# Performance work log

Hardware: AMD Instinct MI355X
Metric: run time of the kernel (lower is better)

## Reference

```python
import jax, jax.numpy as jnp
import numpy as np

B, T, IN = 64, 512, 3      # batch, stroke timesteps, stroke features
H = 512                    # hidden_dim
K = 10                     # num_gaussian_window
NC = 80                    # num_chars
U = 64                     # char_seq_len


def setup_inputs() -> dict:
    key = jax.random.key(0)
    ks = jax.random.split(key, 8)
    w = lambda k, sh: (jax.random.normal(k, sh, jnp.float32) * 0.05)
    return {
        "strokes": jax.random.normal(ks[0], (B, T, IN), jnp.float32),
        "sentences": jax.random.randint(ks[1], (B, U), 0, NC),
        "sentences_mask": jnp.ones((B, U), jnp.float32),
        # nn.LSTMCell params (gate order i, f, g, o)
        "W_ih": w(ks[2], (4 * H, IN + NC)),
        "W_hh": w(ks[3], (4 * H, H)),
        "b_ih": w(ks[4], (4 * H,)),
        "b_hh": w(ks[5], (4 * H,)),
        # window_layer: Linear(H, 3K)
        "W_win": w(ks[6], (3 * K, H)),
        "b_win": w(ks[7], (3 * K,)),
    }


def reference(strokes, sentences, sentences_mask, W_ih, W_hh, b_ih, b_hh, W_win, b_win):
    Bsz, Tlen, _ = strokes.shape
    Ulen = sentences.shape[-1]
    Hh = W_hh.shape[1]
    Kg = W_win.shape[0] // 3
    NCc = W_ih.shape[1] - strokes.shape[-1]
    dt = strokes.dtype

    # one_hot(sentences) * mask, precomputed once: [B, U, NC]
    C = jax.nn.one_hot(sentences, NCc, dtype=dt) * sentences_mask[..., None]
    u = jnp.arange(Ulen, dtype=dt)  # [U]

    def step(carry, x_t):
        h, c, kappa, w = carry
        inp = jnp.concatenate([x_t, w], axis=-1)              # [B, IN+NC]
        gates = inp @ W_ih.T + b_ih + h @ W_hh.T + b_hh       # [B, 4H]
        i, f, g, o = jnp.split(gates, 4, axis=-1)
        c = jax.nn.sigmoid(f) * c + jax.nn.sigmoid(i) * jnp.tanh(g)
        h = jax.nn.sigmoid(o) * jnp.tanh(c)
        p = h @ W_win.T + b_win                               # [B, 3K]
        a_hat, b_hat, k_hat = jnp.split(p, 3, axis=-1)
        alpha = jnp.exp(a_hat)
        beta = jnp.exp(b_hat)
        kappa = kappa + jnp.exp(k_hat)
        # phi[b,u] = sum_k alpha * exp(-beta * (kappa - u)^2)
        phi = jnp.einsum(
            "bk,bku->bu", alpha,
            jnp.exp(-beta[..., None] * (kappa[..., None] - u) ** 2))
        w = jnp.einsum("bu,bun->bn", phi, C)                  # [B, NC]
        return (h, c, kappa, w), (h, w)

    init = (
        jnp.zeros((Bsz, Hh), dt),
        jnp.zeros((Bsz, Hh), dt),
        jnp.zeros((Bsz, Kg), dt),
        jnp.zeros((Bsz, NCc), dt),
    )
    _, (hs, ws) = jax.lax.scan(step, init, jnp.swapaxes(strokes, 0, 1))
    # time-major -> batch-major: [B, T, H], [B, T, NC]
    return jnp.swapaxes(hs, 0, 1), jnp.swapaxes(ws, 0, 1)
```

## Files before the change

### kernel.cpp

```cpp
#include <hip/hip_runtime.h>
#include <hip/hip_bf16.h>


#define GRID_BLOCKS 64
#define TPB 256

typedef __attribute__((ext_vector_type(8))) __bf16 bf16x8;
typedef __attribute__((ext_vector_type(4))) float f32x4;
typedef __attribute__((ext_vector_type(2))) float f32x2;

struct Smem {
    alignas(16) __bf16 wBf[64 * 104];
    float P[64 * 33];
    float Gt[64 * 33];
    float Al[640];
    float Be[640];
    float Ka[640];
    float Wacc[64 * 80];
    float Xt[192];
    float Maskv[4096];
    float Wx[96];
    float Bsum[32];
    float Bwin[32];
    int   Act[64];
    unsigned char Sent[4096];
};

__device__ __forceinline__ float sigf(float x) {
    return 1.f / (1.f + __expf(-x));
}
__device__ __forceinline__ float tanh_fast(float x) {
    float xx = fminf(fmaxf(x, -15.f), 15.f);
    float e = __expf(2.f * xx);
    return (e - 1.f) / (e + 1.f);
}

__global__ void init_ws_kernel(int* ws) {
    int idx = blockIdx.x * TPB + threadIdx.x;
    if (idx < 32832) ws[idx] = 0;
}

__global__ void __launch_bounds__(TPB, 1) lstm_attn(
    const float* __restrict__ strokes,
    const int*   __restrict__ sentences,
    const float* __restrict__ smask,
    const float* __restrict__ Wih,
    const float* __restrict__ Whh,
    const float* __restrict__ bih,
    const float* __restrict__ bhh,
    const float* __restrict__ Wwin,
    const float* __restrict__ bwin,
    float* __restrict__ out,
    unsigned short* __restrict__ hbuf,
    int* __restrict__ flags)
{
    __shared__ Smem S;
    const int tid  = threadIdx.x;
    const int blk  = blockIdx.x;
    const int lane = tid & 63;
    const int wave = tid >> 6;
    const int lm   = lane & 15;
    const int quad = lane >> 4;
    const int myb  = wave * 16 + lm;
    const int koff = quad * 8;
    volatile int* vflags = (volatile int*)flags;

    bf16x8 rbG[2][19];
    bf16x8 rbP[2][16];
    #pragma unroll
    for (int tau = 0; tau < 2; ++tau) {
        const int colg = (lm >> 2) * 512 + blk * 8 + tau * 4 + (lm & 3);
        const float* wr = Whh + colg * 512;
        #pragma unroll
        for (int kc = 0; kc < 16; ++kc) {
            f32x4 lo = *(const f32x4*)(wr + kc * 32 + koff);
            f32x4 hi = *(const f32x4*)(wr + kc * 32 + koff + 4);
            bf16x8 b;
            b[0] = (__bf16)lo[0]; b[1] = (__bf16)lo[1];
            b[2] = (__bf16)lo[2]; b[3] = (__bf16)lo[3];
            b[4] = (__bf16)hi[0]; b[5] = (__bf16)hi[1];
            b[6] = (__bf16)hi[2]; b[7] = (__bf16)hi[3];
            rbG[tau][kc] = b;
        }
        #pragma unroll
        for (int kc = 0; kc < 3; ++kc) {
            bf16x8 b;
            #pragma unroll
            for (int j = 0; j < 8; ++j) {
                int k = kc * 32 + koff + j;
                b[j] = (__bf16)((k < 80) ? Wih[colg * 83 + 3 + k] : 0.f);
            }
            rbG[tau][16 + kc] = b;
        }
    }
    #pragma unroll
    for (int nt = 0; nt < 2; ++nt) {
        const int r = nt * 16 + lm;
        #pragma unroll
        for (int kc = 0; kc < 16; ++kc) {
            bf16x8 b;
            if (r < 30) {
                f32x4 lo = *(const f32x4*)(Wwin + r * 512 + kc * 32 + koff);
                f32x4 hi = *(const f32x4*)(Wwin + r * 512 + kc * 32 + koff + 4);
                b[0] = (__bf16)lo[0]; b[1] = (__bf16)lo[1];
                b[2] = (__bf16)lo[2]; b[3] = (__bf16)lo[3];
                b[4] = (__bf16)hi[0]; b[5] = (__bf16)hi[1];
                b[6] = (__bf16)hi[2]; b[7] = (__bf16)hi[3];
            } else {
                #pragma unroll
                for (int j = 0; j < 8; ++j) b[j] = (__bf16)0.f;
            }
            rbP[nt][kc] = b;
        }
    }

    for (int idx = tid; idx < 4096; idx += TPB) {
        S.Sent[idx]  = (unsigned char)sentences[idx];
        S.Maskv[idx] = smask[idx];
    }
    if (tid < 32) {
        int tau = tid >> 4, m = tid & 15;
        int colg = (m >> 2) * 512 + blk * 8 + tau * 4 + (m & 3);
        S.Bsum[tid] = bih[colg] + bhh[colg];
        S.Wx[tid * 3 + 0] = Wih[colg * 83 + 0];
        S.Wx[tid * 3 + 1] = Wih[colg * 83 + 1];
        S.Wx[tid * 3 + 2] = Wih[colg * 83 + 2];
        S.Bwin[tid] = (tid < 30) ? bwin[tid] : 0.f;
    }
    for (int idx = tid; idx < 640; idx += TPB) S.Ka[idx] = 0.f;
    for (int idx = tid; idx < 5120; idx += TPB) S.Wacc[idx] = 0.f;
    for (int idx = tid; idx < 64 * 104; idx += TPB) S.wBf[idx] = (__bf16)0.f;
    float cst0 = 0.f, cst1 = 0.f;
    __syncthreads();

    const float bs0 = S.Bsum[lm], bs1 = S.Bsum[16 + lm];
    const float bw0 = S.Bwin[lm], bw1 = S.Bwin[16 + lm];
    float wx[6];
    #pragma unroll
    for (int m = 0; m < 3; ++m) {
        wx[m]     = S.Wx[lm * 3 + m];
        wx[3 + m] = S.Wx[(16 + lm) * 3 + m];
    }
    const int pb  = wave * 16 + (lane >> 2);
    const int pa2 = lane & 3;
    bool waccDirty = false;

    for (int t = 0; t <= 512; ++t) {
        if (t >= 1) {
            while (!__all(vflags[lane] >= t)) { }
        }
        const unsigned short* hb = hbuf + ((t + 1) & 1) * 32768 + myb * 512 + koff;
        f32x4 h0,h1,h2,h3,h4,h5,h6,h7,h8,h9,h10,h11,h12,h13,h14,h15;
        asm volatile(
            "global_load_dwordx4 %0, %16, off sc0 sc1\n\t"
            "global_load_dwordx4 %1, %16, off offset:64 sc0 sc1\n\t"
            "global_load_dwordx4 %2, %16, off offset:128 sc0 sc1\n\t"
            "global_load_dwordx4 %3, %16, off offset:192 sc0 sc1\n\t"
            "global_load_dwordx4 %4, %16, off offset:256 sc0 sc1\n\t"
            "global_load_dwordx4 %5, %16, off offset:320 sc0 sc1\n\t"
            "global_load_dwordx4 %6, %16, off offset:384 sc0 sc1\n\t"
            "global_load_dwordx4 %7, %16, off offset:448 sc0 sc1\n\t"
            "global_load_dwordx4 %8, %16, off offset:512 sc0 sc1\n\t"
            "global_load_dwordx4 %9, %16, off offset:576 sc0 sc1\n\t"
            "global_load_dwordx4 %10, %16, off offset:640 sc0 sc1\n\t"
            "global_load_dwordx4 %11, %16, off offset:704 sc0 sc1\n\t"
            "global_load_dwordx4 %12, %16, off offset:768 sc0 sc1\n\t"
            "global_load_dwordx4 %13, %16, off offset:832 sc0 sc1\n\t"
            "global_load_dwordx4 %14, %16, off offset:896 sc0 sc1\n\t"
            "global_load_dwordx4 %15, %16, off offset:960 sc0 sc1\n\t"
            "s_waitcnt vmcnt(0)"
            : "=&v"(h0), "=&v"(h1), "=&v"(h2), "=&v"(h3),
              "=&v"(h4), "=&v"(h5), "=&v"(h6), "=&v"(h7),
              "=&v"(h8), "=&v"(h9), "=&v"(h10), "=&v"(h11),
              "=&v"(h12), "=&v"(h13), "=&v"(h14), "=&v"(h15)
            : "v"(hb)
            : "memory");

        if (t < 512 && lane < 48) {
            int gi = wave * 48 + lane;
            S.Xt[gi] = strokes[(gi / 3) * 1536 + t * 3 + (gi % 3)];
        }

        f32x4 accG0 = {bs0, bs0, bs0, bs0};
        f32x4 accG1 = {bs1, bs1, bs1, bs1};
        f32x4 accP0 = {0.f, 0.f, 0.f, 0.f};
        f32x4 accP1 = {0.f, 0.f, 0.f, 0.f};
        #define KSTEP(R, I) { bf16x8 a = __builtin_bit_cast(bf16x8, R); \
            accP0 = __builtin_amdgcn_mfma_f32_16x16x32_bf16(a, rbP[0][I], accP0, 0, 0, 0); \
            accP1 = __builtin_amdgcn_mfma_f32_16x16x32_bf16(a, rbP[1][I], accP1, 0, 0, 0); \
            accG0 = __builtin_amdgcn_mfma_f32_16x16x32_bf16(a, rbG[0][I], accG0, 0, 0, 0); \
            accG1 = __builtin_amdgcn_mfma_f32_16x16x32_bf16(a, rbG[1][I], accG1, 0, 0, 0); }
        KSTEP(h0, 0)  KSTEP(h1, 1)  KSTEP(h2, 2)  KSTEP(h3, 3)
        KSTEP(h4, 4)  KSTEP(h5, 5)  KSTEP(h6, 6)  KSTEP(h7, 7)
        KSTEP(h8, 8)  KSTEP(h9, 9)  KSTEP(h10, 10) KSTEP(h11, 11)
        KSTEP(h12, 12) KSTEP(h13, 13) KSTEP(h14, 14) KSTEP(h15, 15)
        #undef KSTEP

        #pragma unroll
        for (int r = 0; r < 4; ++r) {
            int row = wave * 16 + quad * 4 + r;
            S.P[row * 33 + lm]      = accP0[r] + bw0;
            S.P[row * 33 + 16 + lm] = accP1[r] + bw1;
        }
        __builtin_amdgcn_wave_barrier();

        bool waveAny = false;
        if (t >= 1) {
            if (lane < 16) S.Act[wave * 16 + lane] = 0;
            __builtin_amdgcn_wave_barrier();
            #pragma unroll
            for (int it = 0; it < 3; ++it) {
                int idx = lane + it * 64;
                if (idx < 160) {
                    int bl = idx / 10, k = idx - bl * 10;
                    int gb = wave * 16 + bl, ad = gb * 10 + k;
                    float ka = S.Ka[ad] + __expf(S.P[gb * 33 + 20 + k]);
                    S.Ka[ad] = ka;
                    S.Al[ad] = __expf(S.P[gb * 33 + k]);
                    float be = __expf(S.P[gb * 33 + 10 + k]);
                    S.Be[ad] = be;
                    float dmin = fmaxf(fmaxf(-ka, ka - 63.f), 0.f);
                    if (be * dmin * dmin <= 36.f) atomicOr(&S.Act[gb], 1);
                }
            }
            __builtin_amdgcn_wave_barrier();
            int actv = (lane < 16) ? S.Act[wave * 16 + lane] : 0;
            waveAny = __any(actv != 0);
            if (waccDirty) {
                for (int i = lane; i < 1280; i += 64) S.Wacc[wave * 1280 + i] = 0.f;
            }
            __builtin_amdgcn_wave_barrier();
            if (waveAny) {
                #pragma unroll 1
                for (int ii = 0; ii < 16; ++ii) {
                    int gb = wave * 16 + ii;
                    if (!S.Act[gb]) continue;
                    float uu = (float)lane;
                    float s = 0.f;
                    #pragma unroll
                    for (int k = 0; k < 10; ++k) {
                        float d = S.Ka[gb * 10 + k] - uu;
                        s = fmaf(S.Al[gb * 10 + k], __expf(-S.Be[gb * 10 + k] * d * d), s);
                    }
                    float val = s * S.Maskv[gb * 64 + lane];
                    if (val != 0.f)
                        atomicAdd(&S.Wacc[gb * 80 + (int)S.Sent[gb * 64 + lane]], val);
                }
            }
            __builtin_amdgcn_wave_barrier();
            if (waveAny || waccDirty) {
                for (int i = lane; i < 1280; i += 64) {
                    int bl = i / 80, n = i - bl * 80;
                    S.wBf[(wave * 16 + bl) * 104 + n] = (__bf16)S.Wacc[wave * 1280 + i];
                }
            }
            __builtin_amdgcn_wave_barrier();
        }

        float hv0 = 0.f, hv1 = 0.f;
        if (t < 512) {
            if (waveAny) {
                const __bf16* wrow = S.wBf + myb * 104 + koff;
                #pragma unroll
                for (int kc = 0; kc < 3; ++kc) {
                    bf16x8 a = *(const bf16x8*)(wrow + kc * 32);
                    accG0 = __builtin_amdgcn_mfma_f32_16x16x32_bf16(a, rbG[0][16 + kc], accG0, 0, 0, 0);
                    accG1 = __builtin_amdgcn_mfma_f32_16x16x32_bf16(a, rbG[1][16 + kc], accG1, 0, 0, 0);
                }
            }
            #pragma unroll
            for (int r = 0; r < 4; ++r) {
                int row = wave * 16 + quad * 4 + r;
                float x0 = S.Xt[row * 3 + 0], x1 = S.Xt[row * 3 + 1], x2 = S.Xt[row * 3 + 2];
                S.Gt[row * 33 + lm]      = accG0[r] + x0 * wx[0] + x1 * wx[1] + x2 * wx[2];
                S.Gt[row * 33 + 16 + lm] = accG1[r] + x0 * wx[3] + x1 * wx[4] + x2 * wx[5];
            }
            __builtin_amdgcn_wave_barrier();
            {
                const float* g = &S.Gt[pb * 33];
                {
                    int c = 2 * pa2, tau = c >> 2, mm = c & 3;
                    const float* gg = g + tau * 16;
                    float cc = sigf(gg[4 + mm]) * cst0 + sigf(gg[mm]) * tanh_fast(gg[8 + mm]);
                    cst0 = cc;
                    hv0 = sigf(gg[12 + mm]) * tanh_fast(cc);
                }
                {
                    int c = 2 * pa2 + 1, tau = c >> 2, mm = c & 3;
                    const float* gg = g + tau * 16;
                    float cc = sigf(gg[4 + mm]) * cst1 + sigf(gg[mm]) * tanh_fast(gg[8 + mm]);
                    cst1 = cc;
                    hv1 = sigf(gg[12 + mm]) * tanh_fast(cc);
                }
                union { __bf16 q[2]; unsigned u; } pk;
                pk.q[0] = (__bf16)hv0; pk.q[1] = (__bf16)hv1;
                ((volatile unsigned*)hbuf)[(t & 1) * 16384 + pb * 256 + blk * 4 + pa2] = pk.u;
            }
        }
        waccDirty = waveAny;

        if (t < 512) {
            __syncthreads();
            if (tid == 0) vflags[blk] = t + 1;
            f32x2 ho = {hv0, hv1};
            *(f32x2*)(out + pb * 262144 + t * 512 + blk * 8 + 2 * pa2) = ho;
        }
        if (t >= 1 && wave == (blk >> 4)) {
            for (int n = lane; n < 80; n += 64)
                out[16777216 + blk * 40960 + (t - 1) * 80 + n] = S.Wacc[blk * 80 + n];
        }
    }
}

extern "C" void kernel_launch(void* const* d_in, const int* in_sizes, int n_in,
                              void* d_out, int out_size, void* d_ws, size_t ws_size,
                              hipStream_t stream) {
    const float* strokes   = (const float*)d_in[0];
    const int*   sentences = (const int*)d_in[1];
    const float* smask     = (const float*)d_in[2];
    const float* Wih       = (const float*)d_in[3];
    const float* Whh       = (const float*)d_in[4];
    const float* bih       = (const float*)d_in[5];
    const float* bhh       = (const float*)d_in[6];
    const float* Wwin      = (const float*)d_in[7];
    const float* bwin      = (const float*)d_in[8];
    float* out = (float*)d_out;
    unsigned short* hbuf = (unsigned short*)d_ws;
    int* flags = (int*)((char*)d_ws + 131072);

    init_ws_kernel<<<129, TPB, 0, stream>>>((int*)d_ws);
    lstm_attn<<<GRID_BLOCKS, TPB, 0, stream>>>(strokes, sentences, smask, Wih, Whh,
                                               bih, bhh, Wwin, bwin, out, hbuf, flags);
}
```

Before: 4.231 ms.

## Use per-wave release flags with single-wave polling and prefetch next stroke input

Replaces the per-block end-of-step __syncthreads plus single flag write with per-wave flags, each written right after that wave's h store drains. Only wave 0 polls all 256 flags, laid out as one 64-byte line per block and read as int4 per lane, with s_sleep between polls, and then releases the other waves through a block barrier. The stroke input for the next step is prefetched into a double-buffered LDS slot, so it is no longer a global load on the critical path. This is meant to shorten the grid-wide step-to-step latency chain, at the cost of a barrier after polling and more flag traffic.

```diff
diff --git a/kernel.cpp b/kernel.cpp
--- a/kernel.cpp
+++ b/kernel.cpp
@@ -8,6 +8,7 @@
 typedef __attribute__((ext_vector_type(8))) __bf16 bf16x8;
 typedef __attribute__((ext_vector_type(4))) float f32x4;
 typedef __attribute__((ext_vector_type(2))) float f32x2;
+typedef __attribute__((ext_vector_type(4))) int i32x4;
 
 struct Smem {
     alignas(16) __bf16 wBf[64 * 104];
@@ -17,7 +18,7 @@
     float Be[640];
     float Ka[640];
     float Wacc[64 * 80];
-    float Xt[192];
+    float Xt[2 * 192];
     float Maskv[4096];
     float Wx[96];
     float Bsum[32];
@@ -37,7 +38,7 @@
 
 __global__ void init_ws_kernel(int* ws) {
     int idx = blockIdx.x * TPB + threadIdx.x;
-    if (idx < 32832) ws[idx] = 0;
+    if (idx < 33792) ws[idx] = 0;
 }
 
 __global__ void __launch_bounds__(TPB, 1) lstm_attn(
@@ -63,7 +64,6 @@
     const int quad = lane >> 4;
     const int myb  = wave * 16 + lm;
     const int koff = quad * 8;
-    volatile int* vflags = (volatile int*)flags;
 
     bf16x8 rbG[2][19];
     bf16x8 rbP[2][16];
@@ -130,6 +130,7 @@
     for (int idx = tid; idx < 640; idx += TPB) S.Ka[idx] = 0.f;
     for (int idx = tid; idx < 5120; idx += TPB) S.Wacc[idx] = 0.f;
     for (int idx = tid; idx < 64 * 104; idx += TPB) S.wBf[idx] = (__bf16)0.f;
+    if (tid < 192) S.Xt[tid] = strokes[(tid / 3) * 1536 + (tid % 3)];
     float cst0 = 0.f, cst1 = 0.f;
     __syncthreads();
 
@@ -147,7 +148,19 @@
 
     for (int t = 0; t <= 512; ++t) {
         if (t >= 1) {
-            while (!__all(vflags[lane] >= t)) { }
+            if (wave == 0) {
+                const volatile i32x4* vf =
+                    (const volatile i32x4*)((const char*)flags + lane * 64);
+                for (;;) {
+                    i32x4 v = *vf;
+                    int m01 = v.x < v.y ? v.x : v.y;
+                    int m23 = v.z < v.w ? v.z : v.w;
+                    int mm  = m01 < m23 ? m01 : m23;
+                    if (__all(mm >= t)) break;
+                    __builtin_amdgcn_s_sleep(1);
+                }
+            }
+            __syncthreads();
         }
         const unsigned short* hb = hbuf + ((t + 1) & 1) * 32768 + myb * 512 + koff;
         f32x4 h0,h1,h2,h3,h4,h5,h6,h7,h8,h9,h10,h11,h12,h13,h14,h15;
@@ -176,11 +189,6 @@
             : "v"(hb)
             : "memory");
 
-        if (t < 512 && lane < 48) {
-            int gi = wave * 48 + lane;
-            S.Xt[gi] = strokes[(gi / 3) * 1536 + t * 3 + (gi % 3)];
-        }
-
         f32x4 accG0 = {bs0, bs0, bs0, bs0};
         f32x4 accG1 = {bs1, bs1, bs1, bs1};
         f32x4 accP0 = {0.f, 0.f, 0.f, 0.f};
@@ -268,10 +276,11 @@
                     accG1 = __builtin_amdgcn_mfma_f32_16x16x32_bf16(a, rbG[1][16 + kc], accG1, 0, 0, 0);
                 }
             }
+            const float* xb = &S.Xt[(t & 1) * 192];
             #pragma unroll
             for (int r = 0; r < 4; ++r) {
                 int row = wave * 16 + quad * 4 + r;
-                float x0 = S.Xt[row * 3 + 0], x1 = S.Xt[row * 3 + 1], x2 = S.Xt[row * 3 + 2];
+                float x0 = xb[row * 3 + 0], x1 = xb[row * 3 + 1], x2 = xb[row * 3 + 2];
                 S.Gt[row * 33 + lm]      = accG0[r] + x0 * wx[0] + x1 * wx[1] + x2 * wx[2];
                 S.Gt[row * 33 + 16 + lm] = accG1[r] + x0 * wx[3] + x1 * wx[4] + x2 * wx[5];
             }
@@ -296,15 +305,22 @@
                 pk.q[0] = (__bf16)hv0; pk.q[1] = (__bf16)hv1;
                 ((volatile unsigned*)hbuf)[(t & 1) * 16384 + pb * 256 + blk * 4 + pa2] = pk.u;
             }
+            asm volatile("s_waitcnt vmcnt(0)" ::: "memory");
+            if (lane == 0)
+                *(volatile int*)((char*)flags + blk * 64 + wave * 4) = t + 1;
+            {
+                f32x2 ho = {hv0, hv1};
+                *(f32x2*)(out + pb * 262144 + t * 512 + blk * 8 + 2 * pa2) = ho;
+            }
+            if (wave != 0 && t + 1 < 512) {
+                int gi = (wave - 1) * 64 + lane;
+                if (gi < 192)
+                    S.Xt[((t + 1) & 1) * 192 + gi] =
+                        strokes[(gi / 3) * 1536 + (t + 1) * 3 + (gi % 3)];
+            }
         }
         waccDirty = waveAny;
 
-        if (t < 512) {
-            __syncthreads();
-            if (tid == 0) vflags[blk] = t + 1;
-            f32x2 ho = {hv0, hv1};
-            *(f32x2*)(out + pb * 262144 + t * 512 + blk * 8 + 2 * pa2) = ho;
-        }
         if (t >= 1 && wave == (blk >> 4)) {
             for (int n = lane; n < 80; n += 64)
                 out[16777216 + blk * 40960 + (t - 1) * 80 + n] = S.Wacc[blk * 80 + n];
@@ -328,7 +344,7 @@
     unsigned short* hbuf = (unsigned short*)d_ws;
     int* flags = (int*)((char*)d_ws + 131072);
 
-    init_ws_kernel<<<129, TPB, 0, stream>>>((int*)d_ws);
+    init_ws_kernel<<<132, TPB, 0, stream>>>((int*)d_ws);
     lstm_attn<<<GRID_BLOCKS, TPB, 0, stream>>>(strokes, sentences, smask, Wih, Whh,
                                                bih, bhh, Wwin, bwin, out, hbuf, flags);
 }
```

Result: faster. 3.810 ms (-10.0%).
